# Performance work log

Hardware: AMD Instinct MI355X
Metric: run time of the kernel (lower is better)

Reference implementation:

```python
import jax, jax.numpy as jnp
import numpy as np
import math

B, S, D, H = 1, 2048, 4096, 32
HD = D // H  # 128
BASE = 10000.0
NEG = -1e9


def rotate_half(x):
    x1, x2 = x[..., : x.shape[-1] // 2], x[..., x.shape[-1] // 2 :]
    return jnp.concatenate((-x2, x1), axis=-1)


def setup_inputs() -> dict:
    key = jax.random.key(0)
    ks = jax.random.split(key, 5)
    scale = 1.0 / math.sqrt(D)
    hidden_states = jax.random.normal(ks[0], (B, S, D), dtype=jnp.float32)
    Wq = jax.random.normal(ks[1], (D, D), dtype=jnp.float32) * scale
    Wk = jax.random.normal(ks[2], (D, D), dtype=jnp.float32) * scale
    Wv = jax.random.normal(ks[3], (D, D), dtype=jnp.float32) * scale
    Wo = jax.random.normal(ks[4], (D, D), dtype=jnp.float32) * scale
    # causal additive mask [1,1,S,S]
    causal = jnp.tril(jnp.ones((S, S), dtype=bool))
    attention_mask = jnp.where(causal, 0.0, NEG).astype(jnp.float32)[None, None]
    # rotary cos/sin cache [1,1,S,HD]
    inv_freq = 1.0 / (BASE ** (jnp.arange(0, HD, 2, dtype=jnp.float32) / HD))
    freqs = jnp.arange(S, dtype=jnp.float32)[:, None] * inv_freq[None, :]
    emb = jnp.concatenate((freqs, freqs), axis=-1)
    cos = jnp.cos(emb)[None, None]
    sin = jnp.sin(emb)[None, None]
    return dict(hidden_states=hidden_states, attention_mask=attention_mask,
                cos=cos, sin=sin, Wq=Wq, Wk=Wk, Wv=Wv, Wo=Wo)


def reference(hidden_states, attention_mask, cos, sin, Wq, Wk, Wv, Wo):
    b, s, d = hidden_states.shape
    # projections (torch Linear: x @ W.T), reshape to [B,H,S,HD]
    def proj(W):
        return (hidden_states @ W.T).reshape(b, s, H, HD).transpose(0, 2, 1, 3)
    q, k, v = proj(Wq), proj(Wk), proj(Wv)
    # RoPE
    q = q * cos + rotate_half(q) * sin
    k = k * cos + rotate_half(k) * sin
    # scores [B,H,S,S], key pre-scaled as in original
    scores = jnp.einsum('bhqd,bhkd->bhqk', q, k / math.sqrt(HD)) + attention_mask
    attn = jax.nn.softmax(scores.astype(jnp.float32), axis=-1).astype(scores.dtype)
    out = jnp.einsum('bhqk,bhkd->bhqd', attn, v)
    out = out.transpose(0, 2, 1, 3).reshape(b, s, d)
    return out @ Wo.T
```

## Files before the change

### kernel.cpp

```cpp
#include <hip/hip_runtime.h>
#include <hip/hip_bf16.h>
#include <stdint.h>

#define DEV __device__ __forceinline__

typedef __bf16 bf16x8 __attribute__((ext_vector_type(8)));
typedef float f32x4 __attribute__((ext_vector_type(4)));
typedef unsigned short ushort8_t __attribute__((ext_vector_type(8)));
typedef unsigned short ushort4_t __attribute__((ext_vector_type(4)));

constexpr int S = 2048;
constexpr int D = 4096;
constexpr int H = 32;
constexpr int HD = 128;
constexpr float kSc = 0.08838834764831845f * 1.4426950408889634f;

DEV unsigned short f2bf(float f) {
    uint32_t u = __builtin_bit_cast(uint32_t, f);
    u += 0x7fffu + ((u >> 16) & 1u);
    return (unsigned short)(u >> 16);
}
DEV float bf2f(unsigned short h) {
    uint32_t u = ((uint32_t)h) << 16;
    return __builtin_bit_cast(float, u);
}

DEV void gload_lds16(const void* g, void* l) {
    __builtin_amdgcn_global_load_lds(
        (const __attribute__((address_space(1))) void*)g,
        (__attribute__((address_space(3))) void*)l,
        16, 0, 0);
}

DEV f32x4 mfma16(bf16x8 a, bf16x8 b, f32x4 c) {
    return __builtin_amdgcn_mfma_f32_16x16x32_bf16(a, b, c, 0, 0, 0);
}

__global__ __launch_bounds__(256) void cvt_all(const float* __restrict__ hs,
                                               const float* __restrict__ w0,
                                               const float* __restrict__ w1,
                                               const float* __restrict__ w2,
                                               const float* __restrict__ w3,
                                               unsigned short* __restrict__ hsb,
                                               unsigned short* __restrict__ o0,
                                               unsigned short* __restrict__ o1,
                                               unsigned short* __restrict__ o2,
                                               unsigned short* __restrict__ o3) {
    const int b = blockIdx.x;
    const float* in;
    unsigned short* out;
    size_t blk;
    if (b < 4096) {
        in = hs; out = hsb; blk = (size_t)b;
    } else {
        const int i = b - 4096;
        const int w = i >> 13;
        const int r = i & 8191;
        in  = (w == 0) ? w0 : (w == 1) ? w1 : (w == 2) ? w2 : w3;
        out = (w == 0) ? o0 : (w == 1) ? o1 : (w == 2) ? o2 : o3;
        blk = (size_t)r;
    }
    const size_t i8 = blk * 256 + threadIdx.x;
    f32x4 a = ((const f32x4*)in)[2 * i8];
    f32x4 c = ((const f32x4*)in)[2 * i8 + 1];
    ushort8_t o;
    o[0] = f2bf(a[0]); o[1] = f2bf(a[1]); o[2] = f2bf(a[2]); o[3] = f2bf(a[3]);
    o[4] = f2bf(c[0]); o[5] = f2bf(c[1]); o[6] = f2bf(c[2]); o[7] = f2bf(c[3]);
    ((ushort8_t*)out)[i8] = o;
}

template <int BN, int OMODE>
__global__ __launch_bounds__(512, 2) void gemm8(const unsigned short* __restrict__ Ap,
                                                const unsigned short* __restrict__ Bp,
                                                unsigned short* __restrict__ Oq,
                                                unsigned short* __restrict__ Ok,
                                                unsigned short* __restrict__ Ovt,
                                                float* __restrict__ Of) {
    constexpr int NT = BN / 64;
    constexpr int NB = BN / 64;
    extern __shared__ unsigned short lds8[];
    unsigned short (*As)[8192] = (unsigned short(*)[8192])lds8;
    unsigned short* Bs0 = lds8 + 4 * 8192;
    unsigned short* Bs1 = Bs0 + BN * 64;

    const int tix = threadIdx.x;
    const int lane = tix & 63;
    const int w = tix >> 6;
    const int g = lane >> 4;
    const int rl = lane & 15;
    const int wm = w >> 2;
    const int wn = w & 3;
    const int bc0 = wn * (BN / 4);
    const int rx = rl & 7;

    const int yy = blockIdx.x & 7;
    const int xx = blockIdx.x >> 3;
    const int m0 = yy * 256;
    const int n0 = xx * BN;

    int srowA[2], scolA[2];
#pragma unroll
    for (int u = 0; u < 2; ++u) {
        const int c = u * 512 + tix;
        srowA[u] = c >> 3;
        scolA[u] = ((c & 7) ^ (srowA[u] & 7)) << 3;
    }
    int srowB[NB], scolB[NB];
#pragma unroll
    for (int u = 0; u < NB; ++u) {
        const int c = u * 512 + tix;
        srowB[u] = c >> 3;
        scolB[u] = ((c & 7) ^ (srowB[u] & 7)) << 3;
    }

    const char* aBase[2] = {(const char*)As[wm], (const char*)As[2 + wm]};
    const char* bBase[2] = {(const char*)Bs0, (const char*)Bs1};

    f32x4 acc[4][2][NT] = {};
    bf16x8 bfr[NT][2];

#define STG_A8(t, h, slot)                                                        \
    if ((t) < 64) {                                                               \
        _Pragma("unroll") for (int u = 0; u < 2; ++u)                             \
            gload_lds16(Ap + (size_t)(m0 + (h) * 128 + srowA[u]) * 4096 +         \
                            (t) * 64 + scolA[u],                                  \
                        &As[slot][(u * 512 + tix) * 8]);                          \
    }
#define STG_B8(t, slot)                                                           \
    if ((t) < 64) {                                                               \
        unsigned short* bs_ = (slot) ? Bs1 : Bs0;                                 \
        _Pragma("unroll") for (int u = 0; u < NB; ++u)                            \
            gload_lds16(Bp + (size_t)(n0 + srowB[u]) * 4096 +                     \
                            (t) * 64 + scolB[u],                                  \
                        &bs_[(u * 512 + tix) * 8]);                               \
    }

#define PHASE8(pt, q, STG, VM)                                                    \
    {                                                                             \
        bf16x8 af[2][2];                                                          \
        _Pragma("unroll") for (int mi = 0; mi < 2; ++mi)                          \
        _Pragma("unroll") for (int ks = 0; ks < 2; ++ks) {                        \
            const int ab = ((q) * 32 + mi * 16 + rl) * 128 +                      \
                           ((((ks << 2) + g) ^ rx) << 4);                         \
            af[mi][ks] = *(const bf16x8*)(aBase[pt] + ab);                        \
        }                                                                         \
        if ((q) == 0) {                                                           \
            _Pragma("unroll") for (int nt = 0; nt < NT; ++nt)                     \
            _Pragma("unroll") for (int ks = 0; ks < 2; ++ks) {                    \
                const int bb = (bc0 + nt * 16 + rl) * 128 +                       \
                               ((((ks << 2) + g) ^ rx) << 4);                     \
                bfr[nt][ks] = *(const bf16x8*)(bBase[pt] + bb);                   \
            }                                                                     \
        }                                                                         \
        STG;                                                                      \
        if (VM) {                                                                 \
            if (last) {                                                           \
                asm volatile("s_waitcnt vmcnt(0)" ::: "memory");                  \
            } else if constexpr (NB == 3) {                                       \
                asm volatile("s_waitcnt vmcnt(3)" ::: "memory");                  \
            } else {                                                              \
                asm volatile("s_waitcnt vmcnt(2)" ::: "memory");                  \
            }                                                                     \
        }                                                                         \
        __builtin_amdgcn_s_barrier();                                             \
        __builtin_amdgcn_s_setprio(1);                                            \
        _Pragma("unroll") for (int ks = 0; ks < 2; ++ks)                          \
        _Pragma("unroll") for (int mi = 0; mi < 2; ++mi)                          \
        _Pragma("unroll") for (int nt = 0; nt < NT; ++nt)                         \
            acc[q][mi][nt] = mfma16(af[mi][ks], bfr[nt][ks], acc[q][mi][nt]);     \
        __builtin_amdgcn_s_setprio(0);                                            \
        __builtin_amdgcn_s_barrier();                                             \
    }

    STG_A8(0, 0, 0); STG_A8(0, 1, 1);
    STG_B8(0, 0); STG_B8(1, 1);
    __syncthreads();

    for (int i = 0; i < 32; ++i) {
        const bool last = (i == 31);
        const int o = 2 * i + 1, ne = 2 * i + 2, no = 2 * i + 3;
        PHASE8(0, 0, STG_A8(o, 0, 2), 0)
        PHASE8(0, 1, STG_A8(o, 1, 3), 0)
        PHASE8(0, 2, STG_B8(ne, 0), 0)
        PHASE8(0, 3, ((void)0), 1)
        PHASE8(1, 0, STG_A8(ne, 0, 0), 0)
        PHASE8(1, 1, STG_A8(ne, 1, 1), 0)
        PHASE8(1, 2, STG_B8(no, 1), 0)
        PHASE8(1, 3, ((void)0), 1)
    }
#undef PHASE8
#undef STG_A8
#undef STG_B8

#pragma unroll
    for (int q = 0; q < 4; ++q)
#pragma unroll
        for (int mi = 0; mi < 2; ++mi)
#pragma unroll
            for (int nt = 0; nt < NT; ++nt) {
                const int row0 = m0 + wm * 128 + q * 32 + mi * 16 + g * 4;
                const int gc = n0 + bc0 + nt * 16 + rl;
                if constexpr (OMODE == 0) {
                    const int sel = gc >> 12;
                    const int col = gc & 4095;
                    if (sel == 2) {
                        ushort4_t v;
#pragma unroll
                        for (int r = 0; r < 4; ++r) v[r] = f2bf(acc[q][mi][nt][r]);
                        *(ushort4_t*)&Ovt[(size_t)col * S + row0] = v;
                    } else {
                        unsigned short* op = sel ? Ok : Oq;
#pragma unroll
                        for (int r = 0; r < 4; ++r)
                            op[(size_t)(row0 + r) * 4096 + col] = f2bf(acc[q][mi][nt][r]);
                    }
                } else {
#pragma unroll
                    for (int r = 0; r < 4; ++r)
                        Of[(size_t)(row0 + r) * 4096 + gc] = acc[q][mi][nt][r];
                }
            }
}

__global__ __launch_bounds__(256) void rope_kernel(unsigned short* __restrict__ Qb,
                                                   unsigned short* __restrict__ Kb,
                                                   const float* __restrict__ cosT,
                                                   const float* __restrict__ sinT) {
    const int i = blockIdx.x * 256 + threadIdx.x;
    const int j8 = i & 7;
    const int h = (i >> 3) & 31;
    const int s = i >> 8;
    const size_t base = (size_t)s * D + h * HD + j8 * 8;
    const float* cp = cosT + s * HD + j8 * 8;
    const float* sp = sinT + s * HD + j8 * 8;
    float c1[8], s1[8], c2[8], s2[8];
#pragma unroll
    for (int k = 0; k < 8; ++k) { c1[k] = cp[k]; s1[k] = sp[k]; c2[k] = cp[k + 64]; s2[k] = sp[k + 64]; }

#pragma unroll
    for (int w = 0; w < 2; ++w) {
        unsigned short* p = (w == 0 ? Qb : Kb) + base;
        const float f = (w == 0) ? kSc : 1.0f;
        ushort8_t x1 = *(ushort8_t*)p;
        ushort8_t x2 = *(ushort8_t*)(p + 64);
        ushort8_t o1, o2;
#pragma unroll
        for (int k = 0; k < 8; ++k) {
            const float a = bf2f(x1[k]);
            const float b = bf2f(x2[k]);
            o1[k] = f2bf((a * c1[k] - b * s1[k]) * f);
            o2[k] = f2bf((b * c2[k] + a * s2[k]) * f);
        }
        *(ushort8_t*)p = o1;
        *(ushort8_t*)(p + 64) = o2;
    }
}

constexpr int NQT = S / 128;
__global__ __launch_bounds__(256, 2) void flash_attn(const unsigned short* __restrict__ Q,
                                                     const unsigned short* __restrict__ K,
                                                     const unsigned short* __restrict__ V,
                                                     unsigned short* __restrict__ O) {
    __shared__ unsigned short Ks[2][64 * 128];
    __shared__ unsigned short Vs[128 * 64];
    __shared__ unsigned short Ps[4][32 * 64];

    const int t = threadIdx.x;
    const int lane = t & 63;
    const int wid = t >> 6;
    const int g = lane >> 4;
    const int rl = lane & 15;
    const int bid = blockIdx.x;
    const int qt = (NQT - 1) - (bid >> 5);
    const int h = bid & 31;
    const int q0 = qt * 128;
    const int wrow0 = q0 + wid * 32;

    bf16x8 qf[2][4];
#pragma unroll
    for (int mi = 0; mi < 2; ++mi) {
        const unsigned short* qp = Q + (size_t)(wrow0 + mi * 16 + rl) * D + h * HD;
#pragma unroll
        for (int ks = 0; ks < 4; ++ks) qf[mi][ks] = *(const bf16x8*)(qp + ks * 32 + g * 8);
    }

    f32x4 accO[2][8] = {};
    float m2s[2] = {-1e30f, -1e30f};
    float lsum[2] = {0.f, 0.f};

#pragma unroll
    for (int r = 0; r < 4; ++r) {
        const int c = r * 256 + t;
        const int rowk = c >> 4;
        const int srck = (c & 15) ^ (rowk & 7);
        gload_lds16(K + (size_t)rowk * D + h * HD + srck * 8,
                    &Ks[0][(r * 256 + wid * 64) * 8]);
    }
    __syncthreads();

    int cur = 0;
    const int ntiles = 2 * qt + 2;
    for (int kv = 0; kv < ntiles; ++kv) {
        const int kv0 = kv * 64;
#pragma unroll
        for (int r = 0; r < 4; ++r) {
            const int c = r * 256 + t;
            const int rowv = c >> 3;
            const int srcv = (c & 7) ^ (rowv & 7);
            gload_lds16(V + (size_t)(h * HD + rowv) * S + kv0 + srcv * 8,
                        &Vs[(r * 256 + wid * 64) * 8]);
        }
        if (kv + 1 < ntiles) {
#pragma unroll
            for (int r = 0; r < 4; ++r) {
                const int c = r * 256 + t;
                const int rowk = c >> 4;
                const int srck = (c & 15) ^ (rowk & 7);
                gload_lds16(K + (size_t)(kv0 + 64 + rowk) * D + h * HD + srck * 8,
                            &Ks[cur ^ 1][(r * 256 + wid * 64) * 8]);
            }
        }

        const bool active = kv0 <= wrow0 + 31;
        if (active) {
            f32x4 sf[2][4];
#pragma unroll
            for (int mi = 0; mi < 2; ++mi)
#pragma unroll
                for (int nt = 0; nt < 4; ++nt) sf[mi][nt] = f32x4{0.f, 0.f, 0.f, 0.f};
            __builtin_amdgcn_s_setprio(1);
#pragma unroll
            for (int nt = 0; nt < 4; ++nt) {
                const int row = nt * 16 + rl;
#pragma unroll
                for (int ks = 0; ks < 4; ++ks) {
                    bf16x8 kf = *(const bf16x8*)&Ks[cur][row * 128 + (((ks * 4 + g) ^ (row & 7)) << 3)];
                    sf[0][nt] = mfma16(kf, qf[0][ks], sf[0][nt]);
                    sf[1][nt] = mfma16(kf, qf[1][ks], sf[1][nt]);
                }
            }
            __builtin_amdgcn_s_setprio(0);

            const bool needMask = (kv0 + 63 > wrow0);
            float cf2[2];
            bool chg = false;
#pragma unroll
            for (int mi = 0; mi < 2; ++mi) {
                const int qrow = wrow0 + mi * 16 + rl;
                float mx = -1e30f;
                if (needMask) {
#pragma unroll
                    for (int nt = 0; nt < 4; ++nt)
#pragma unroll
                        for (int r = 0; r < 4; ++r) {
                            const int kcol = kv0 + nt * 16 + g * 4 + r;
                            float s = sf[mi][nt][r];
                            s = (kcol > qrow) ? -1e30f : s;
                            sf[mi][nt][r] = s;
                            mx = fmaxf(mx, s);
                        }
                } else {
#pragma unroll
                    for (int nt = 0; nt < 4; ++nt)
#pragma unroll
                        for (int r = 0; r < 4; ++r) mx = fmaxf(mx, sf[mi][nt][r]);
                }
                mx = fmaxf(mx, __shfl_xor(mx, 16));
                mx = fmaxf(mx, __shfl_xor(mx, 32));
                const float mn = fmaxf(m2s[mi], mx);
                cf2[mi] = __builtin_amdgcn_exp2f(m2s[mi] - mn);
                chg |= (mn > m2s[mi]);
                m2s[mi] = mn;
                float rs = 0.f;
#pragma unroll
                for (int nt = 0; nt < 4; ++nt)
#pragma unroll
                    for (int r = 0; r < 4; ++r) {
                        const float p = __builtin_amdgcn_exp2f(sf[mi][nt][r] - mn);
                        sf[mi][nt][r] = p;
                        rs += p;
                    }
                rs += __shfl_xor(rs, 16);
                rs += __shfl_xor(rs, 32);
                lsum[mi] = lsum[mi] * cf2[mi] + rs;
            }

            if (__any((int)chg)) {
#pragma unroll
                for (int mi = 0; mi < 2; ++mi)
#pragma unroll
                    for (int nt = 0; nt < 8; ++nt)
#pragma unroll
                        for (int r = 0; r < 4; ++r) accO[mi][nt][r] *= cf2[mi];
            }

            unsigned short* myP = Ps[wid];
#pragma unroll
            for (int mi = 0; mi < 2; ++mi) {
                const int row = mi * 16 + rl;
                const int rxp = row & 7;
#pragma unroll
                for (int nt = 0; nt < 4; ++nt) {
                    ushort4_t v;
#pragma unroll
                    for (int r = 0; r < 4; ++r) v[r] = f2bf(sf[mi][nt][r]);
                    const int chunk = nt * 2 + (g >> 1);
                    *(ushort4_t*)&myP[row * 64 + ((chunk ^ rxp) << 3) + ((g & 1) << 2)] = v;
                }
            }
        }
        __syncthreads();

        if (active) {
            unsigned short* myP = Ps[wid];
            __builtin_amdgcn_s_setprio(1);
#pragma unroll
            for (int ks = 0; ks < 2; ++ks) {
                bf16x8 pa[2];
#pragma unroll
                for (int mi = 0; mi < 2; ++mi) {
                    const int row = mi * 16 + rl;
                    pa[mi] = *(const bf16x8*)&myP[row * 64 + (((ks * 4 + g) ^ (row & 7)) << 3)];
                }
#pragma unroll
                for (int nt = 0; nt < 8; ++nt) {
                    const int vrow = nt * 16 + rl;
                    bf16x8 vf = *(const bf16x8*)&Vs[vrow * 64 + (((ks * 4 + g) ^ (vrow & 7)) << 3)];
                    accO[0][nt] = mfma16(vf, pa[0], accO[0][nt]);
                    accO[1][nt] = mfma16(vf, pa[1], accO[1][nt]);
                }
            }
            __builtin_amdgcn_s_setprio(0);
        }
        __syncthreads();
        cur ^= 1;
    }

#pragma unroll
    for (int mi = 0; mi < 2; ++mi) {
        const float inv = 1.0f / lsum[mi];
        const int qrow = wrow0 + mi * 16 + rl;
#pragma unroll
        for (int nt = 0; nt < 8; ++nt) {
            ushort4_t v;
#pragma unroll
            for (int r = 0; r < 4; ++r) v[r] = f2bf(accO[mi][nt][r] * inv);
            *(ushort4_t*)&O[(size_t)qrow * D + h * HD + nt * 16 + g * 4] = v;
        }
    }
}

extern "C" void kernel_launch(void* const* d_in, const int* in_sizes, int n_in,
                              void* d_out, int out_size, void* d_ws, size_t ws_size,
                              hipStream_t stream) {
    const float* hs   = (const float*)d_in[0];
    const float* cosT = (const float*)d_in[2];
    const float* sinT = (const float*)d_in[3];
    const float* Wq   = (const float*)d_in[4];
    const float* Wk   = (const float*)d_in[5];
    const float* Wv   = (const float*)d_in[6];
    const float* Wo   = (const float*)d_in[7];

    char* ws = (char*)d_ws;
    const size_t MB = 1ull << 20;
    unsigned short* hsb = (unsigned short*)(ws);
    unsigned short* wqb = (unsigned short*)(ws + 16 * MB);
    unsigned short* wkb = (unsigned short*)(ws + 48 * MB);
    unsigned short* wvb = (unsigned short*)(ws + 80 * MB);
    unsigned short* wob = (unsigned short*)(ws + 112 * MB);
    unsigned short* Qb  = (unsigned short*)(ws + 144 * MB);
    unsigned short* Kb  = (unsigned short*)(ws + 160 * MB);
    unsigned short* Vt  = (unsigned short*)(ws + 176 * MB);
    unsigned short* AOb = (unsigned short*)(ws + 192 * MB);

    cvt_all<<<4096 + 4 * 8192, 256, 0, stream>>>(hs, Wq, Wk, Wv, Wo,
                                                 hsb, wqb, wkb, wvb, wob);

    gemm8<192, 0><<<512, 512, 114688, stream>>>(hsb, wqb, Qb, Kb, Vt, nullptr);

    rope_kernel<<<2048, 256, 0, stream>>>(Qb, Kb, cosT, sinT);

    flash_attn<<<dim3(NQT * H), 256, 0, stream>>>(Qb, Kb, Vt, AOb);

    gemm8<128, 1><<<256, 512, 98304, stream>>>(AOb, wob, nullptr, nullptr, nullptr,
                                               (float*)d_out);
}
```

Before: 417.8 us.

## Pair complementary causal query tiles per block and use lazy softmax max rescaling

The flash attention kernel now runs 512-thread blocks. Each block pairs query tile 8+p with tile 7-p for one head, so every block does the same amount of causal work and they share the K/V tile loads through LDS, held in a larger dynamic shared buffer. It also skips updating the running max unless the new max exceeds the old one by more than 8 (in log2 units), which reduces how often the accumulator is rescaled. The grid drops to 256 blocks. This risks lower occupancy and idle waves in the short-tile half once their causal range ends, and the lazy max allows probabilities up to 2^8 before normalisation.

```diff
diff --git a/kernel.cpp b/kernel.cpp
--- a/kernel.cpp
+++ b/kernel.cpp
@@ -256,14 +256,14 @@
     }
 }
 
-constexpr int NQT = S / 128;
-__global__ __launch_bounds__(256, 2) void flash_attn(const unsigned short* __restrict__ Q,
+__global__ __launch_bounds__(512, 2) void flash_attn(const unsigned short* __restrict__ Q,
                                                      const unsigned short* __restrict__ K,
                                                      const unsigned short* __restrict__ V,
                                                      unsigned short* __restrict__ O) {
-    __shared__ unsigned short Ks[2][64 * 128];
-    __shared__ unsigned short Vs[128 * 64];
-    __shared__ unsigned short Ps[4][32 * 64];
+    extern __shared__ unsigned short ldsA[];
+    unsigned short* KsB = ldsA;
+    unsigned short* VsB = ldsA + 16384;
+    unsigned short* PsB = ldsA + 24576;
 
     const int t = threadIdx.x;
     const int lane = t & 63;
@@ -271,10 +271,10 @@
     const int g = lane >> 4;
     const int rl = lane & 15;
     const int bid = blockIdx.x;
-    const int qt = (NQT - 1) - (bid >> 5);
+    const int p = 7 - (bid >> 5);
     const int h = bid & 31;
-    const int q0 = qt * 128;
-    const int wrow0 = q0 + wid * 32;
+    const int qt = (wid < 4) ? (8 + p) : (7 - p);
+    const int wrow0 = qt * 128 + (wid & 3) * 32;
 
     bf16x8 qf[2][4];
 #pragma unroll
@@ -289,40 +289,39 @@
     float lsum[2] = {0.f, 0.f};
 
 #pragma unroll
-    for (int r = 0; r < 4; ++r) {
-        const int c = r * 256 + t;
+    for (int r = 0; r < 2; ++r) {
+        const int c = r * 512 + t;
         const int rowk = c >> 4;
         const int srck = (c & 15) ^ (rowk & 7);
-        gload_lds16(K + (size_t)rowk * D + h * HD + srck * 8,
-                    &Ks[0][(r * 256 + wid * 64) * 8]);
+        gload_lds16(K + (size_t)rowk * D + h * HD + srck * 8, &KsB[c * 8]);
     }
     __syncthreads();
 
     int cur = 0;
-    const int ntiles = 2 * qt + 2;
+    const int ntiles = 2 * (8 + p) + 2;
     for (int kv = 0; kv < ntiles; ++kv) {
         const int kv0 = kv * 64;
 #pragma unroll
-        for (int r = 0; r < 4; ++r) {
-            const int c = r * 256 + t;
+        for (int r = 0; r < 2; ++r) {
+            const int c = r * 512 + t;
             const int rowv = c >> 3;
             const int srcv = (c & 7) ^ (rowv & 7);
-            gload_lds16(V + (size_t)(h * HD + rowv) * S + kv0 + srcv * 8,
-                        &Vs[(r * 256 + wid * 64) * 8]);
+            gload_lds16(V + (size_t)(h * HD + rowv) * S + kv0 + srcv * 8, &VsB[c * 8]);
         }
         if (kv + 1 < ntiles) {
 #pragma unroll
-            for (int r = 0; r < 4; ++r) {
-                const int c = r * 256 + t;
+            for (int r = 0; r < 2; ++r) {
+                const int c = r * 512 + t;
                 const int rowk = c >> 4;
                 const int srck = (c & 15) ^ (rowk & 7);
                 gload_lds16(K + (size_t)(kv0 + 64 + rowk) * D + h * HD + srck * 8,
-                            &Ks[cur ^ 1][(r * 256 + wid * 64) * 8]);
+                            &KsB[(cur ^ 1) * 8192 + c * 8]);
             }
         }
 
         const bool active = kv0 <= wrow0 + 31;
         if (active) {
+            const unsigned short* KsC = KsB + cur * 8192;
             f32x4 sf[2][4];
 #pragma unroll
             for (int mi = 0; mi < 2; ++mi)
@@ -334,7 +333,7 @@
                 const int row = nt * 16 + rl;
 #pragma unroll
                 for (int ks = 0; ks < 4; ++ks) {
-                    bf16x8 kf = *(const bf16x8*)&Ks[cur][row * 128 + (((ks * 4 + g) ^ (row & 7)) << 3)];
+                    bf16x8 kf = *(const bf16x8*)&KsC[row * 128 + (((ks * 4 + g) ^ (row & 7)) << 3)];
                     sf[0][nt] = mfma16(kf, qf[0][ks], sf[0][nt]);
                     sf[1][nt] = mfma16(kf, qf[1][ks], sf[1][nt]);
                 }
@@ -367,7 +366,7 @@
                 }
                 mx = fmaxf(mx, __shfl_xor(mx, 16));
                 mx = fmaxf(mx, __shfl_xor(mx, 32));
-                const float mn = fmaxf(m2s[mi], mx);
+                const float mn = (mx <= m2s[mi] + 8.f) ? m2s[mi] : mx;
                 cf2[mi] = __builtin_amdgcn_exp2f(m2s[mi] - mn);
                 chg |= (mn > m2s[mi]);
                 m2s[mi] = mn;
@@ -376,9 +375,9 @@
                 for (int nt = 0; nt < 4; ++nt)
 #pragma unroll
                     for (int r = 0; r < 4; ++r) {
-                        const float p = __builtin_amdgcn_exp2f(sf[mi][nt][r] - mn);
-                        sf[mi][nt][r] = p;
-                        rs += p;
+                        const float pv = __builtin_amdgcn_exp2f(sf[mi][nt][r] - mn);
+                        sf[mi][nt][r] = pv;
+                        rs += pv;
                     }
                 rs += __shfl_xor(rs, 16);
                 rs += __shfl_xor(rs, 32);
@@ -394,7 +393,7 @@
                         for (int r = 0; r < 4; ++r) accO[mi][nt][r] *= cf2[mi];
             }
 
-            unsigned short* myP = Ps[wid];
+            unsigned short* myP = PsB + wid * 2048;
 #pragma unroll
             for (int mi = 0; mi < 2; ++mi) {
                 const int row = mi * 16 + rl;
@@ -412,7 +411,7 @@
         __syncthreads();
 
         if (active) {
-            unsigned short* myP = Ps[wid];
+            unsigned short* myP = PsB + wid * 2048;
             __builtin_amdgcn_s_setprio(1);
 #pragma unroll
             for (int ks = 0; ks < 2; ++ks) {
@@ -425,7 +424,7 @@
 #pragma unroll
                 for (int nt = 0; nt < 8; ++nt) {
                     const int vrow = nt * 16 + rl;
-                    bf16x8 vf = *(const bf16x8*)&Vs[vrow * 64 + (((ks * 4 + g) ^ (vrow & 7)) << 3)];
+                    bf16x8 vf = *(const bf16x8*)&VsB[vrow * 64 + (((ks * 4 + g) ^ (vrow & 7)) << 3)];
                     accO[0][nt] = mfma16(vf, pa[0], accO[0][nt]);
                     accO[1][nt] = mfma16(vf, pa[1], accO[1][nt]);
                 }
@@ -480,7 +479,7 @@
 
     rope_kernel<<<2048, 256, 0, stream>>>(Qb, Kb, cosT, sinT);
 
-    flash_attn<<<dim3(NQT * H), 256, 0, stream>>>(Qb, Kb, Vt, AOb);
+    flash_attn<<<256, 512, 81920, stream>>>(Qb, Kb, Vt, AOb);
 
     gemm8<128, 1><<<256, 512, 98304, stream>>>(AOb, wob, nullptr, nullptr, nullptr,
                                                (float*)d_out);
```

After: 414.3 us. No clear change (-0.8%).
